# Performance work log

Hardware: AMD Instinct MI355X
Metric: run time of the kernel (lower is better)

Reference implementation:

```python
import jax, jax.numpy as jnp
import numpy as np

UNITS = 65
BATCH = 50
SEQ = 8192


def setup_inputs() -> dict:
    key = jax.random.key(0)
    ks = jax.random.split(key, 6)
    x = jax.random.normal(ks[0], (BATCH, SEQ, UNITS), dtype=jnp.float32)
    # Single shared LSTM cell (same cell object reused for all 3 stacked layers)
    W = jax.random.normal(ks[1], (UNITS, 4 * UNITS), dtype=jnp.float32) * 0.1
    U = jax.random.normal(ks[2], (UNITS, 4 * UNITS), dtype=jnp.float32) * 0.1
    b = jax.random.normal(ks[3], (4 * UNITS,), dtype=jnp.float32) * 0.1
    # Dense output projection 65 -> 65
    Wd = jax.random.normal(ks[4], (UNITS, UNITS), dtype=jnp.float32) * 0.1
    bd = jax.random.normal(ks[5], (UNITS,), dtype=jnp.float32) * 0.1
    return {"x": x, "W": W, "U": U, "b": b, "Wd": Wd, "bd": bd}


def _lstm_cell(x_t, h, c, W, U, b):
    # Keras LSTMCell: gates in order i, f, g(candidate), o
    z = x_t @ W + h @ U + b                      # [B, 4*units]
    i, f, g, o = jnp.split(z, 4, axis=-1)
    i = jax.nn.sigmoid(i)
    f = jax.nn.sigmoid(f)
    g = jnp.tanh(g)
    o = jax.nn.sigmoid(o)
    c_new = f * c + i * g
    h_new = o * jnp.tanh(c_new)
    return h_new, c_new


def reference(x, W, U, b, Wd, bd):
    B = x.shape[0]
    zeros = jnp.zeros((B, UNITS), dtype=x.dtype)
    init = (zeros, zeros, zeros, zeros, zeros, zeros)  # (h1,c1,h2,c2,h3,c3)

    def step(carry, x_t):
        h1, c1, h2, c2, h3, c3 = carry
        h1, c1 = _lstm_cell(x_t, h1, c1, W, U, b)  # layer 1 (shared weights)
        h2, c2 = _lstm_cell(h1, h2, c2, W, U, b)   # layer 2 (shared weights)
        h3, c3 = _lstm_cell(h2, h3, c3, W, U, b)   # layer 3 (shared weights)
        return (h1, c1, h2, c2, h3, c3), h3

    xs = jnp.swapaxes(x, 0, 1)                   # [T, B, 65]
    _, ys = jax.lax.scan(step, init, xs)         # ys: [T, B, 65]
    ys = jnp.swapaxes(ys, 0, 1)                  # [B, T, 65]
    out = ys @ Wd + bd                           # dense projection to vocab 65
    return out
```

## Files before the change

### kernel.cpp

```cpp
#include <hip/hip_runtime.h>

#define UNITS 65
#define SEQ   8192
#define BATCH 50

__device__ __forceinline__ float frcp(float x){ return __builtin_amdgcn_rcpf(x); }
__device__ __forceinline__ float fsigmoid(float x){ return frcp(1.0f + __expf(-x)); }
__device__ __forceinline__ float ftanh(float x){
    float e2 = __expf(2.0f * x);
    return 1.0f - 2.0f * frcp(e2 + 1.0f);
}

template<int CTRL>
__device__ __forceinline__ float dppadd(float x){
    int t = __builtin_amdgcn_update_dpp(0, __float_as_int(x), CTRL, 0xF, 0xF, true);
    return x + __int_as_float(t);
}
template<int CTRL>
__device__ __forceinline__ float dppmov(float x){
    int t = __builtin_amdgcn_update_dpp(0, __float_as_int(x), CTRL, 0xF, 0xF, true);
    return __int_as_float(t);
}
__device__ __forceinline__ float red4_all(float x){
    x = dppadd<0xB1>(x);
    x = dppadd<0x4E>(x);
    return x;
}
__device__ __forceinline__ float red16_lane15(float x){
    x = dppadd<0x111>(x);
    x = dppadd<0x112>(x);
    x = dppadd<0x114>(x);
    x = dppadd<0x118>(x);
    return x;
}
__device__ __forceinline__ void bar_lds(){
    asm volatile("s_waitcnt lgkmcnt(0)\n\ts_barrier" ::: "memory");
}
__device__ __forceinline__ float rdlane(float v, int l){
    return __int_as_float(__builtin_amdgcn_readlane(__float_as_int(v), l));
}

__device__ __forceinline__ int inpos(int k){
    int q = k >> 5; if (q > 3) q = 3;
    return q * 36 + (k - (q << 5));
}
__device__ __forceinline__ float wrow(const float* W, const float* U, int k, int c){
    return (k < 65) ? W[k * 260 + c] : U[(k - 65) * 260 + c];
}


#define LOADVV(vv, base) do {                                                  \
    const float* vp_ = (base) + kq * 36;                                       \
    _Pragma("unroll")                                                          \
    for (int q8_ = 0; q8_ < 8; ++q8_) {                                        \
        float4 f_ = *(const float4*)(vp_ + 4 * q8_);                           \
        vv[4*q8_+0] = f_.x; vv[4*q8_+1] = f_.y;                                \
        vv[4*q8_+2] = f_.z; vv[4*q8_+3] = f_.w;                                \
    }                                                                          \
    { float2 f2_ = *(const float2*)(vp_ + 32); vv[32] = f2_.x; vv[33] = f2_.y; } \
} while (0)

#define LAYERB(aI, aF, aG, aO, CST, ...) do {                                  \
    float rI_ = red4_all(aI), rF_ = red4_all(aF);                              \
    float rG_ = red4_all(aG), rO_ = red4_all(aO);                              \
    float z_ = ((kq == 0) ? rI_ : (kq == 1) ? rF_ : (kq == 2) ? rG_ : rO_) + breg; \
    float sg_ = frcp(1.0f + __expf(-sk * z_));                                 \
    float g_  = fmaf(sk, sg_, dk);                                             \
    float gi_ = dppmov<0x00>(g_);                                              \
    float gf_ = dppmov<0x55>(g_);                                              \
    float gg_ = dppmov<0xAA>(g_);                                              \
    float cn_ = fmaf(gf_, CST, gi_ * gg_);                                     \
    float hn_ = g_ * ftanh(cn_);                                               \
    if (wr) { CST = cn_; __VA_ARGS__; }                                        \
} while (0)

#define STEP(L0, L1, L2) do {                                                  \
    const float* __restrict__ vbase = &vbuf[cur][0][0];                        \
    float*       __restrict__ nbase = &vbuf[cur ^ 1][0][0];                    \
         \
    float xq1 = 0.0f, ex1 = 0.0f;                                              \
    if (L0) {                                                                  \
        const int tl_ = (s + 2 < SEQ) ? (s + 2) : (SEQ - 1);                   \
        if (wr) xq1 = xrow[(size_t)tl_ * UNITS + j];                           \
        if (wave == 1 && lane == 0) ex1 = xrow[(size_t)tl_ * UNITS + 64];      \
    }                                                                          \
            \
    float vv0[34], vv1[34], vv2[34];                                           \
    if (L0) LOADVV(vv0, vbase);                                                \
    if (L1) LOADVV(vv1, vbase + 144);                                          \
    if (L2) LOADVV(vv2, vbase + 288);                                          \
        \
    const float* vm_ = vbase + ml * 144;                                       \
    float4 uA_ = *(const float4*)(vm_ + p64);                                  \
    float4 uB_ = *(const float4*)(vm_ + p64 + 4);                              \
    float  uex_ = (i64 < 2) ? vm_[140 + i64] : 0.0f;                           \
                   \
    float aI0=0,aF0=0,aG0=0,aO0=0, aI1=0,aF1=0,aG1=0,aO1=0,                    \
          aI2=0,aF2=0,aG2=0,aO2=0;                                             \
    _Pragma("unroll")                                                          \
    for (int kk = 0; kk < 34; ++kk) {                                          \
        if (L0) { float s0_ = vv0[kk];                                         \
            aI0=fmaf(s0_,wI[kk],aI0); aF0=fmaf(s0_,wF[kk],aF0);                \
            aG0=fmaf(s0_,wG[kk],aG0); aO0=fmaf(s0_,wO[kk],aO0); }              \
        if (L1) { float s1_ = vv1[kk];                                         \
            aI1=fmaf(s1_,wI[kk],aI1); aF1=fmaf(s1_,wF[kk],aF1);                \
            aG1=fmaf(s1_,wG[kk],aG1); aO1=fmaf(s1_,wO[kk],aO1); }              \
        if (L2) { float s2_ = vv2[kk];                                         \
            aI2=fmaf(s2_,wI[kk],aI2); aF2=fmaf(s2_,wF[kk],aF2);                \
            aG2=fmaf(s2_,wG[kk],aG2); aO2=fmaf(s2_,wO[kk],aO2); }              \
    }                                                                          \
                           \
    float a64_ = uA_.x * w64[0];                                               \
    a64_ = fmaf(uA_.y, w64[1], a64_); a64_ = fmaf(uA_.z, w64[2], a64_);        \
    a64_ = fmaf(uA_.w, w64[3], a64_); a64_ = fmaf(uB_.x, w64[4], a64_);        \
    a64_ = fmaf(uB_.y, w64[5], a64_); a64_ = fmaf(uB_.z, w64[6], a64_);        \
    a64_ = fmaf(uB_.w, w64[7], a64_); a64_ = fmaf(uex_, w64x, a64_);           \
    a64_ = red16_lane15(a64_);                                                 \
                                            \
    if (L0) LAYERB(aI0, aF0, aG0, aO0, c1,                                     \
                   nbase[ipH] = hn_; nbase[144 + ipI] = hn_);                  \
    if (L1) LAYERB(aI1, aF1, aG1, aO1, c2,                                     \
                   nbase[144 + ipH] = hn_; nbase[288 + ipI] = hn_);            \
    if (L2) LAYERB(aI2, aF2, aG2, aO2, c3,                                     \
                   nbase[288 + ipH] = hn_;                                     \
                   orow[(size_t)(s - 2) * UNITS + j] = hn_);                   \
    if (L0) { if (wr) { nbase[ipI] = xq0; xq0 = xq1; } }                       \
                               \
    {                                                                          \
        const bool act64_ = (wave == 1) ? (bool)(L0)                           \
                          : (wave == 2) ? (bool)(L1)                           \
                          : (wave == 3) ? (bool)(L2) : false;                  \
        float zi_ = rdlane(a64_, 15) + b64i;                                   \
        float zf_ = rdlane(a64_, 31) + b64f;                                   \
        float zg_ = rdlane(a64_, 47) + b64g;                                   \
        float zo_ = rdlane(a64_, 63) + b64o;                                   \
        float gi4_ = fsigmoid(zi_), gf4_ = fsigmoid(zf_);                      \
        float gg4_ = ftanh(zg_),    go4_ = fsigmoid(zo_);                      \
        float cn64_ = fmaf(gf4_, c64, gi4_ * gg4_);                            \
        float hn64_ = go4_ * ftanh(cn64_);                                     \
        if (act64_) {                                                          \
            c64 = cn64_;                                                       \
            if (lane == 0) {                                                   \
                nbase[ml * 144 + 141] = hn64_;                                 \
                if (wave <= 2) nbase[wave * 144 + 72] = hn64_;                 \
                else orow[(size_t)(s - 2) * UNITS + 64] = hn64_;               \
            }                                                                  \
            if (wave == 1) { if (lane == 0) nbase[72] = ex0; ex0 = ex1; }      \
        }                                                                      \
    }                                                                          \
    cur ^= 1;                                                                  \
    bar_lds();                                                                 \
} while (0)

__global__ __launch_bounds__(256, 1)
void lstm3_kernel(const float* __restrict__ x, const float* __restrict__ W,
                  const float* __restrict__ U, const float* __restrict__ b,
                  float* __restrict__ out)
{
    const int e    = blockIdx.x;
    const int tid  = threadIdx.x;
    const int wave = tid >> 6, lane = tid & 63;
    const int kq   = lane & 3, jl = lane >> 2;
    const int j    = wave * 16 + jl;
    const bool wr  = (kq == 3);

    __shared__ __attribute__((aligned(16))) float vbuf[2][3][144];

    float wI[34], wF[34], wG[34], wO[34];
    #pragma unroll
    for (int kk = 0; kk < 34; ++kk) {
        int k = kq * 32 + kk;
        wI[kk] = wrow(W, U, k, j);
        wF[kk] = wrow(W, U, k, 65  + j);
        wG[kk] = wrow(W, U, k, 130 + j);
        wO[kk] = wrow(W, U, k, 195 + j);
    }
    const float breg = b[kq * 65 + j];
    const float sk   = (kq == 2) ? 2.0f : 1.0f;
    const float dk   = 1.0f - sk;

    const int i64 = lane & 15, g64 = lane >> 4;
    const int p64 = (i64 >> 2) * 36 + 8 * (i64 & 3);
    float w64[8], w64x;
    {
        const int c64 = g64 * 65 + 64;
        #pragma unroll
        for (int r = 0; r < 8; ++r) w64[r] = wrow(W, U, 8 * i64 + r, c64);
        w64x = (i64 < 2) ? wrow(W, U, 128 + i64, c64) : 0.0f;
    }
    const float b64i = b[64], b64f = b[129], b64g = b[194], b64o = b[259];
    const int ml = (wave == 0) ? 0 : wave - 1;

    float c1 = 0, c2 = 0, c3 = 0, c64 = 0;

    const float* xrow = x   + (size_t)e * SEQ * UNITS;
    float*       orow = out + (size_t)e * SEQ * UNITS;
    const int ipI = inpos(j), ipH = inpos(65 + j);

    for (int i = tid; i < 2 * 3 * 144; i += 256) ((float*)vbuf)[i] = 0.0f;
    __syncthreads();
    if (wr)  vbuf[0][0][ipI] = xrow[j];
    if (wave == 1 && lane == 0) vbuf[0][0][72] = xrow[64];
    __syncthreads();

    float xq0 = 0, ex0 = 0;
    if (wr) xq0 = xrow[UNITS + j];
    if (wave == 1 && lane == 0) ex0 = xrow[UNITS + 64];

    int cur = 0;
    int s = 0;
    STEP(1, 0, 0); ++s;
    STEP(1, 1, 0); ++s;
    for (; s < SEQ; ++s) { STEP(1, 1, 1); }
    STEP(0, 1, 1); ++s;
    STEP(0, 0, 1);
}

__global__ __launch_bounds__(256)
void dense_kernel(float* __restrict__ io,
                  const float* __restrict__ Wd,
                  const float* __restrict__ bd)
{
    __shared__ __attribute__((aligned(16))) float wS[65 * 68];
    __shared__ float bS[65];
    for (int i = threadIdx.x; i < 65 * 65; i += 256) {
        int r = i / 65, c = i - r * 65;
        wS[r * 68 + c] = Wd[i];
    }
    if (threadIdx.x < 65) bS[threadIdx.x] = bd[threadIdx.x];
    __syncthreads();

    const size_t row  = (size_t)blockIdx.x * 256 + threadIdx.x;
    const size_t base = row * 65;

    float r[65];
    #pragma unroll
    for (int k = 0; k < 65; ++k) r[k] = io[base + k];

    for (int ct = 0; ct < 16; ++ct) {
        const int c = ct * 4;
        float a0 = bS[c], a1 = bS[c + 1], a2 = bS[c + 2], a3 = bS[c + 3];
        #pragma unroll
        for (int k = 0; k < 65; ++k) {
            const float4 wv = *reinterpret_cast<const float4*>(&wS[k * 68 + c]);
            a0 += r[k] * wv.x;
            a1 += r[k] * wv.y;
            a2 += r[k] * wv.z;
            a3 += r[k] * wv.w;
        }
        io[base + c]     = a0;
        io[base + c + 1] = a1;
        io[base + c + 2] = a2;
        io[base + c + 3] = a3;
    }
    float a = bS[64];
    #pragma unroll
    for (int k = 0; k < 65; ++k) a += r[k] * wS[k * 68 + 64];
    io[base + 64] = a;
}

extern "C" void kernel_launch(void* const* d_in, const int* in_sizes, int n_in,
                              void* d_out, int out_size, void* d_ws, size_t ws_size,
                              hipStream_t stream)
{
    const float* x  = (const float*)d_in[0];
    const float* W  = (const float*)d_in[1];
    const float* U  = (const float*)d_in[2];
    const float* b  = (const float*)d_in[3];
    const float* Wd = (const float*)d_in[4];
    const float* bd = (const float*)d_in[5];
    float* out = (float*)d_out;

    hipLaunchKernelGGL(lstm3_kernel, dim3(BATCH), dim3(256), 0, stream, x, W, U, b, out);
    hipLaunchKernelGGL(dense_kernel, dim3(1600), dim3(256), 0, stream, out, Wd, bd);
}
```

Before: 15.23 ms.

## Pack two batch sequences per 512-thread block and stream LDS loads into FMA loop

Each block now runs two independent batch elements, eight waves sharing one barrier, with separate LDS double buffers per element. The grid is halved to 25 blocks. The per-step vector loads are moved inside the FMA loop as float4 chunks instead of being staged into 34-element register arrays, which cuts register pressure so two waves fit per SIMD. The cost is that each barrier now waits on both sequences, and launch_bounds(512,2) may force register spills given the ~136 weight registers per thread.

```diff
diff --git a/kernel.cpp b/kernel.cpp
--- a/kernel.cpp
+++ b/kernel.cpp
@@ -48,17 +48,6 @@
     return (k < 65) ? W[k * 260 + c] : U[(k - 65) * 260 + c];
 }
 
-
-#define LOADVV(vv, base) do {                                                  \
-    const float* vp_ = (base) + kq * 36;                                       \
-    _Pragma("unroll")                                                          \
-    for (int q8_ = 0; q8_ < 8; ++q8_) {                                        \
-        float4 f_ = *(const float4*)(vp_ + 4 * q8_);                           \
-        vv[4*q8_+0] = f_.x; vv[4*q8_+1] = f_.y;                                \
-        vv[4*q8_+2] = f_.z; vv[4*q8_+3] = f_.w;                                \
-    }                                                                          \
-    { float2 f2_ = *(const float2*)(vp_ + 32); vv[32] = f2_.x; vv[33] = f2_.y; } \
-} while (0)
 
 #define LAYERB(aI, aF, aG, aO, CST, ...) do {                                  \
     float rI_ = red4_all(aI), rF_ = red4_all(aF);                              \
@@ -75,39 +64,64 @@
 } while (0)
 
 #define STEP(L0, L1, L2) do {                                                  \
-    const float* __restrict__ vbase = &vbuf[cur][0][0];                        \
-    float*       __restrict__ nbase = &vbuf[cur ^ 1][0][0];                    \
-         \
+    const float* __restrict__ vbase = &vbuf[eh][cur][0][0];                    \
+    float*       __restrict__ nbase = &vbuf[eh][cur ^ 1][0][0];                \
+           \
     float xq1 = 0.0f, ex1 = 0.0f;                                              \
     if (L0) {                                                                  \
         const int tl_ = (s + 2 < SEQ) ? (s + 2) : (SEQ - 1);                   \
         if (wr) xq1 = xrow[(size_t)tl_ * UNITS + j];                           \
-        if (wave == 1 && lane == 0) ex1 = xrow[(size_t)tl_ * UNITS + 64];      \
-    }                                                                          \
-            \
-    float vv0[34], vv1[34], vv2[34];                                           \
-    if (L0) LOADVV(vv0, vbase);                                                \
-    if (L1) LOADVV(vv1, vbase + 144);                                          \
-    if (L2) LOADVV(vv2, vbase + 288);                                          \
-        \
+        if (wave4 == 1 && lane == 0) ex1 = xrow[(size_t)tl_ * UNITS + 64];     \
+    }                                                                          \
+     \
     const float* vm_ = vbase + ml * 144;                                       \
     float4 uA_ = *(const float4*)(vm_ + p64);                                  \
     float4 uB_ = *(const float4*)(vm_ + p64 + 4);                              \
     float  uex_ = (i64 < 2) ? vm_[140 + i64] : 0.0f;                           \
-                   \
+     \
+    const float* vp0_ = vbase + kq * 36;                                       \
+    const float* vp1_ = vbase + 144 + kq * 36;                                 \
+    const float* vp2_ = vbase + 288 + kq * 36;                                 \
     float aI0=0,aF0=0,aG0=0,aO0=0, aI1=0,aF1=0,aG1=0,aO1=0,                    \
           aI2=0,aF2=0,aG2=0,aO2=0;                                             \
     _Pragma("unroll")                                                          \
-    for (int kk = 0; kk < 34; ++kk) {                                          \
-        if (L0) { float s0_ = vv0[kk];                                         \
-            aI0=fmaf(s0_,wI[kk],aI0); aF0=fmaf(s0_,wF[kk],aF0);                \
-            aG0=fmaf(s0_,wG[kk],aG0); aO0=fmaf(s0_,wO[kk],aO0); }              \
-        if (L1) { float s1_ = vv1[kk];                                         \
-            aI1=fmaf(s1_,wI[kk],aI1); aF1=fmaf(s1_,wF[kk],aF1);                \
-            aG1=fmaf(s1_,wG[kk],aG1); aO1=fmaf(s1_,wO[kk],aO1); }              \
-        if (L2) { float s2_ = vv2[kk];                                         \
-            aI2=fmaf(s2_,wI[kk],aI2); aF2=fmaf(s2_,wF[kk],aF2);                \
-            aG2=fmaf(s2_,wG[kk],aG2); aO2=fmaf(s2_,wO[kk],aO2); }              \
+    for (int q8_ = 0; q8_ < 8; ++q8_) {                                        \
+        float4 f0_, f1_, f2_;                                                  \
+        if (L0) f0_ = *(const float4*)(vp0_ + 4 * q8_);                        \
+        if (L1) f1_ = *(const float4*)(vp1_ + 4 * q8_);                        \
+        if (L2) f2_ = *(const float4*)(vp2_ + 4 * q8_);                        \
+        _Pragma("unroll")                                                      \
+        for (int r_ = 0; r_ < 4; ++r_) {                                       \
+            const int kk = 4 * q8_ + r_;                                       \
+            if (L0) { float s0_ = (&f0_.x)[r_];                                \
+                aI0=fmaf(s0_,wI[kk],aI0); aF0=fmaf(s0_,wF[kk],aF0);            \
+                aG0=fmaf(s0_,wG[kk],aG0); aO0=fmaf(s0_,wO[kk],aO0); }          \
+            if (L1) { float s1_ = (&f1_.x)[r_];                                \
+                aI1=fmaf(s1_,wI[kk],aI1); aF1=fmaf(s1_,wF[kk],aF1);            \
+                aG1=fmaf(s1_,wG[kk],aG1); aO1=fmaf(s1_,wO[kk],aO1); }          \
+            if (L2) { float s2_ = (&f2_.x)[r_];                                \
+                aI2=fmaf(s2_,wI[kk],aI2); aF2=fmaf(s2_,wF[kk],aF2);            \
+                aG2=fmaf(s2_,wG[kk],aG2); aO2=fmaf(s2_,wO[kk],aO2); }          \
+        }                                                                      \
+    }                                                                          \
+    {                                                     \
+        float2 t0_, t1_, t2_;                                                  \
+        if (L0) t0_ = *(const float2*)(vp0_ + 32);                             \
+        if (L1) t1_ = *(const float2*)(vp1_ + 32);                             \
+        if (L2) t2_ = *(const float2*)(vp2_ + 32);                             \
+        _Pragma("unroll")                                                      \
+        for (int r_ = 0; r_ < 2; ++r_) {                                       \
+            const int kk = 32 + r_;                                            \
+            if (L0) { float s0_ = (&t0_.x)[r_];                                \
+                aI0=fmaf(s0_,wI[kk],aI0); aF0=fmaf(s0_,wF[kk],aF0);            \
+                aG0=fmaf(s0_,wG[kk],aG0); aO0=fmaf(s0_,wO[kk],aO0); }          \
+            if (L1) { float s1_ = (&t1_.x)[r_];                                \
+                aI1=fmaf(s1_,wI[kk],aI1); aF1=fmaf(s1_,wF[kk],aF1);            \
+                aG1=fmaf(s1_,wG[kk],aG1); aO1=fmaf(s1_,wO[kk],aO1); }          \
+            if (L2) { float s2_ = (&t2_.x)[r_];                                \
+                aI2=fmaf(s2_,wI[kk],aI2); aF2=fmaf(s2_,wF[kk],aF2);            \
+                aG2=fmaf(s2_,wG[kk],aG2); aO2=fmaf(s2_,wO[kk],aO2); }          \
+        }                                                                      \
     }                                                                          \
                            \
     float a64_ = uA_.x * w64[0];                                               \
@@ -127,9 +141,9 @@
     if (L0) { if (wr) { nbase[ipI] = xq0; xq0 = xq1; } }                       \
                                \
     {                                                                          \
-        const bool act64_ = (wave == 1) ? (bool)(L0)                           \
-                          : (wave == 2) ? (bool)(L1)                           \
-                          : (wave == 3) ? (bool)(L2) : false;                  \
+        const bool act64_ = (wave4 == 1) ? (bool)(L0)                          \
+                          : (wave4 == 2) ? (bool)(L1)                          \
+                          : (wave4 == 3) ? (bool)(L2) : false;                 \
         float zi_ = rdlane(a64_, 15) + b64i;                                   \
         float zf_ = rdlane(a64_, 31) + b64f;                                   \
         float zg_ = rdlane(a64_, 47) + b64g;                                   \
@@ -142,29 +156,30 @@
             c64 = cn64_;                                                       \
             if (lane == 0) {                                                   \
                 nbase[ml * 144 + 141] = hn64_;                                 \
-                if (wave <= 2) nbase[wave * 144 + 72] = hn64_;                 \
+                if (wave4 <= 2) nbase[wave4 * 144 + 72] = hn64_;               \
                 else orow[(size_t)(s - 2) * UNITS + 64] = hn64_;               \
             }                                                                  \
-            if (wave == 1) { if (lane == 0) nbase[72] = ex0; ex0 = ex1; }      \
+            if (wave4 == 1) { if (lane == 0) nbase[72] = ex0; ex0 = ex1; }     \
         }                                                                      \
     }                                                                          \
     cur ^= 1;                                                                  \
     bar_lds();                                                                 \
 } while (0)
 
-__global__ __launch_bounds__(256, 1)
+__global__ __launch_bounds__(512, 2)
 void lstm3_kernel(const float* __restrict__ x, const float* __restrict__ W,
                   const float* __restrict__ U, const float* __restrict__ b,
                   float* __restrict__ out)
 {
-    const int e    = blockIdx.x;
-    const int tid  = threadIdx.x;
-    const int wave = tid >> 6, lane = tid & 63;
-    const int kq   = lane & 3, jl = lane >> 2;
-    const int j    = wave * 16 + jl;
-    const bool wr  = (kq == 3);
-
-    __shared__ __attribute__((aligned(16))) float vbuf[2][3][144];
+    const int tid   = threadIdx.x;
+    const int wave  = tid >> 6, lane = tid & 63;
+    const int eh    = wave >> 2, wave4 = wave & 3;
+    const int e     = blockIdx.x * 2 + eh;
+    const int kq    = lane & 3, jl = lane >> 2;
+    const int j     = wave4 * 16 + jl;
+    const bool wr   = (kq == 3);
+
+    __shared__ __attribute__((aligned(16))) float vbuf[2][2][3][144];
 
     float wI[34], wF[34], wG[34], wO[34];
     #pragma unroll
@@ -189,7 +204,7 @@
         w64x = (i64 < 2) ? wrow(W, U, 128 + i64, c64) : 0.0f;
     }
     const float b64i = b[64], b64f = b[129], b64g = b[194], b64o = b[259];
-    const int ml = (wave == 0) ? 0 : wave - 1;
+    const int ml = (wave4 == 0) ? 0 : wave4 - 1;
 
     float c1 = 0, c2 = 0, c3 = 0, c64 = 0;
 
@@ -197,15 +212,15 @@
     float*       orow = out + (size_t)e * SEQ * UNITS;
     const int ipI = inpos(j), ipH = inpos(65 + j);
 
-    for (int i = tid; i < 2 * 3 * 144; i += 256) ((float*)vbuf)[i] = 0.0f;
+    for (int i = tid; i < 2 * 2 * 3 * 144; i += 512) ((float*)&vbuf[0][0][0][0])[i] = 0.0f;
     __syncthreads();
-    if (wr)  vbuf[0][0][ipI] = xrow[j];
-    if (wave == 1 && lane == 0) vbuf[0][0][72] = xrow[64];
+    if (wr)  vbuf[eh][0][0][ipI] = xrow[j];
+    if (wave4 == 1 && lane == 0) vbuf[eh][0][0][72] = xrow[64];
     __syncthreads();
 
     float xq0 = 0, ex0 = 0;
     if (wr) xq0 = xrow[UNITS + j];
-    if (wave == 1 && lane == 0) ex0 = xrow[UNITS + 64];
+    if (wave4 == 1 && lane == 0) ex0 = xrow[UNITS + 64];
 
     int cur = 0;
     int s = 0;
@@ -271,6 +286,6 @@
     const float* bd = (const float*)d_in[5];
     float* out = (float*)d_out;
 
-    hipLaunchKernelGGL(lstm3_kernel, dim3(BATCH), dim3(256), 0, stream, x, W, U, b, out);
+    hipLaunchKernelGGL(lstm3_kernel, dim3(BATCH / 2), dim3(512), 0, stream, x, W, U, b, out);
     hipLaunchKernelGGL(dense_kernel, dim3(1600), dim3(256), 0, stream, out, Wd, bd);
 }
```

Result: slower. 23.89 ms (+56.8%).

## Give each lane a full gate column and broadcast inputs via readlane

Applied to the files above, without the earlier changes.

The gate matmul is reorganised so each lane owns one gate column and keeps all 130 weights in registers. The state vector is read from LDS as one float4 per lane and broadcast with v_readlane, instead of each lane loading 34 values and reducing four partial sums with DPP. The x prefetch and the 65th unit's computation are restructured to match the new LDS layout. This removes the per-lane LDS vector loads and the cross-lane reductions. In exchange it adds about one readlane per FMA, lengthens the dependent FMA chains and raises register pressure.

```diff
diff --git a/kernel.cpp b/kernel.cpp
--- a/kernel.cpp
+++ b/kernel.cpp
@@ -3,6 +3,8 @@
 #define UNITS 65
 #define SEQ   8192
 #define BATCH 50
+#define LW    136
+#define PW    (3 * LW)
 
 __device__ __forceinline__ float frcp(float x){ return __builtin_amdgcn_rcpf(x); }
 __device__ __forceinline__ float fsigmoid(float x){ return frcp(1.0f + __expf(-x)); }
@@ -21,131 +23,115 @@
     int t = __builtin_amdgcn_update_dpp(0, __float_as_int(x), CTRL, 0xF, 0xF, true);
     return __int_as_float(t);
 }
-__device__ __forceinline__ float red4_all(float x){
-    x = dppadd<0xB1>(x);
-    x = dppadd<0x4E>(x);
-    return x;
-}
-__device__ __forceinline__ float red16_lane15(float x){
+__device__ __forceinline__ float red64_63(float x){
     x = dppadd<0x111>(x);
     x = dppadd<0x112>(x);
     x = dppadd<0x114>(x);
     x = dppadd<0x118>(x);
+    x = dppadd<0x142>(x);
+    x = dppadd<0x143>(x);
     return x;
 }
 __device__ __forceinline__ void bar_lds(){
     asm volatile("s_waitcnt lgkmcnt(0)\n\ts_barrier" ::: "memory");
 }
-__device__ __forceinline__ float rdlane(float v, int l){
-    return __int_as_float(__builtin_amdgcn_readlane(__float_as_int(v), l));
-}
-
-__device__ __forceinline__ int inpos(int k){
-    int q = k >> 5; if (q > 3) q = 3;
-    return q * 36 + (k - (q << 5));
-}
+
 __device__ __forceinline__ float wrow(const float* W, const float* U, int k, int c){
     return (k < 65) ? W[k * 260 + c] : U[(k - 65) * 260 + c];
 }
 
-
-#define LOADVV(vv, base) do {                                                  \
-    const float* vp_ = (base) + kq * 36;                                       \
-    _Pragma("unroll")                                                          \
-    for (int q8_ = 0; q8_ < 8; ++q8_) {                                        \
-        float4 f_ = *(const float4*)(vp_ + 4 * q8_);                           \
-        vv[4*q8_+0] = f_.x; vv[4*q8_+1] = f_.y;                                \
-        vv[4*q8_+2] = f_.z; vv[4*q8_+3] = f_.w;                                \
-    }                                                                          \
-    { float2 f2_ = *(const float2*)(vp_ + 32); vv[32] = f2_.x; vv[33] = f2_.y; } \
-} while (0)
-
-#define LAYERB(aI, aF, aG, aO, CST, ...) do {                                  \
-    float rI_ = red4_all(aI), rF_ = red4_all(aF);                              \
-    float rG_ = red4_all(aG), rO_ = red4_all(aO);                              \
-    float z_ = ((kq == 0) ? rI_ : (kq == 1) ? rF_ : (kq == 2) ? rG_ : rO_) + breg; \
+#define VW(K) ((K) < 65 ? (K) : (K) + 3)
+#define RLF(fv, W_) __int_as_float(__builtin_amdgcn_readlane(                   \
+        __float_as_int((&(fv).x)[(W_) & 3]), (W_) >> 2))
+
+
+#define ACT(ZS, CST, ...) do {                                                 \
+    float z_  = (ZS) + breg;                                                   \
     float sg_ = frcp(1.0f + __expf(-sk * z_));                                 \
-    float g_  = fmaf(sk, sg_, dk);                                             \
+    float g_  = fmaf(sk, sg_, dk);            \
     float gi_ = dppmov<0x00>(g_);                                              \
     float gf_ = dppmov<0x55>(g_);                                              \
     float gg_ = dppmov<0xAA>(g_);                                              \
     float cn_ = fmaf(gf_, CST, gi_ * gg_);                                     \
     float hn_ = g_ * ftanh(cn_);                                               \
-    if (wr) { CST = cn_; __VA_ARGS__; }                                        \
+    if (og) { CST = cn_; __VA_ARGS__; }                                        \
 } while (0)
 
 #define STEP(L0, L1, L2) do {                                                  \
-    const float* __restrict__ vbase = &vbuf[cur][0][0];                        \
-    float*       __restrict__ nbase = &vbuf[cur ^ 1][0][0];                    \
-         \
-    float xq1 = 0.0f, ex1 = 0.0f;                                              \
-    if (L0) {                                                                  \
+    float* vb = lds + cur * PW;                                                \
+    float* vn = lds + (cur ^ 1) * PW;                                          \
+              \
+    float4 nx4 = {0,0,0,0}; float nxs = 0.0f;                                  \
+    if (L0) { if (wave == 0) {                                                 \
         const int tl_ = (s + 2 < SEQ) ? (s + 2) : (SEQ - 1);                   \
-        if (wr) xq1 = xrow[(size_t)tl_ * UNITS + j];                           \
-        if (wave == 1 && lane == 0) ex1 = xrow[(size_t)tl_ * UNITS + 64];      \
+        if (lane < 16) nx4 = *(const float4*)(xrow + (size_t)tl_ * UNITS + 4 * lane); \
+        if (lane == 16) nxs = xrow[(size_t)tl_ * UNITS + 64];                  \
+    } }                                                                        \
+                           \
+    float4 fv0 = {0,0,0,0}, fv1 = {0,0,0,0}, fv2 = {0,0,0,0};                  \
+    if (L0) fv0 = *(const float4*)(vb + rdoff);                                \
+    if (L1) fv1 = *(const float4*)(vb + LW + rdoff);                           \
+    if (L2) fv2 = *(const float4*)(vb + 2 * LW + rdoff);                       \
+     \
+    float a0 = 0, a0b = 0, a1 = 0, a1b = 0, a2 = 0, a2b = 0;                   \
+    _Pragma("unroll")                                                          \
+    for (int k = 0; k < 130; ++k) {                                            \
+        if (L0) { float sv_ = RLF(fv0, VW(k));                                 \
+            if (k < 65) a0  = fmaf(sv_, wcol[k], a0);                          \
+            else        a0b = fmaf(sv_, wcol[k], a0b); }                       \
+        if (L1) { float sv_ = RLF(fv1, VW(k));                                 \
+            if (k < 65) a1  = fmaf(sv_, wcol[k], a1);                          \
+            else        a1b = fmaf(sv_, wcol[k], a1b); }                       \
+        if (L2) { float sv_ = RLF(fv2, VW(k));                                 \
+            if (k < 65) a2  = fmaf(sv_, wcol[k], a2);                          \
+            else        a2b = fmaf(sv_, wcol[k], a2b); }                       \
     }                                                                          \
-            \
-    float vv0[34], vv1[34], vv2[34];                                           \
-    if (L0) LOADVV(vv0, vbase);                                                \
-    if (L1) LOADVV(vv1, vbase + 144);                                          \
-    if (L2) LOADVV(vv2, vbase + 288);                                          \
-        \
-    const float* vm_ = vbase + ml * 144;                                       \
-    float4 uA_ = *(const float4*)(vm_ + p64);                                  \
-    float4 uB_ = *(const float4*)(vm_ + p64 + 4);                              \
-    float  uex_ = (i64 < 2) ? vm_[140 + i64] : 0.0f;                           \
-                   \
-    float aI0=0,aF0=0,aG0=0,aO0=0, aI1=0,aF1=0,aG1=0,aO1=0,                    \
-          aI2=0,aF2=0,aG2=0,aO2=0;                                             \
-    _Pragma("unroll")                                                          \
-    for (int kk = 0; kk < 34; ++kk) {                                          \
-        if (L0) { float s0_ = vv0[kk];                                         \
-            aI0=fmaf(s0_,wI[kk],aI0); aF0=fmaf(s0_,wF[kk],aF0);                \
-            aG0=fmaf(s0_,wG[kk],aG0); aO0=fmaf(s0_,wO[kk],aO0); }              \
-        if (L1) { float s1_ = vv1[kk];                                         \
-            aI1=fmaf(s1_,wI[kk],aI1); aF1=fmaf(s1_,wF[kk],aF1);                \
-            aG1=fmaf(s1_,wG[kk],aG1); aO1=fmaf(s1_,wO[kk],aO1); }              \
-        if (L2) { float s2_ = vv2[kk];                                         \
-            aI2=fmaf(s2_,wI[kk],aI2); aF2=fmaf(s2_,wF[kk],aF2);                \
-            aG2=fmaf(s2_,wG[kk],aG2); aO2=fmaf(s2_,wO[kk],aO2); }              \
-    }                                                                          \
-                           \
-    float a64_ = uA_.x * w64[0];                                               \
-    a64_ = fmaf(uA_.y, w64[1], a64_); a64_ = fmaf(uA_.z, w64[2], a64_);        \
-    a64_ = fmaf(uA_.w, w64[3], a64_); a64_ = fmaf(uB_.x, w64[4], a64_);        \
-    a64_ = fmaf(uB_.y, w64[5], a64_); a64_ = fmaf(uB_.z, w64[6], a64_);        \
-    a64_ = fmaf(uB_.w, w64[7], a64_); a64_ = fmaf(uex_, w64x, a64_);           \
-    a64_ = red16_lane15(a64_);                                                 \
-                                            \
-    if (L0) LAYERB(aI0, aF0, aG0, aO0, c1,                                     \
-                   nbase[ipH] = hn_; nbase[144 + ipI] = hn_);                  \
-    if (L1) LAYERB(aI1, aF1, aG1, aO1, c2,                                     \
-                   nbase[144 + ipH] = hn_; nbase[288 + ipI] = hn_);            \
-    if (L2) LAYERB(aI2, aF2, aG2, aO2, c3,                                     \
-                   nbase[288 + ipH] = hn_;                                     \
-                   orow[(size_t)(s - 2) * UNITS + j] = hn_);                   \
-    if (L0) { if (wr) { nbase[ipI] = xq0; xq0 = xq1; } }                       \
-                               \
+           \
+    if (L0) { if (wave == 0) {                                                 \
+        if (lane < 16) *(float4*)(vn + 4 * lane) = xq4;                        \
+        if (lane == 16) vn[64] = xqs;                                          \
+        xq4 = nx4; xqs = nxs;                                                  \
+    } }                                                                        \
+                                                   \
+    if (L0) ACT(a0 + a0b, c_0,                                                 \
+                vn[68 + j] = hn_;                         \
+                vn[LW + j] = hn_);                        \
+    if (L1) ACT(a1 + a1b, c_1,                                                 \
+                vn[LW + 68 + j] = hn_;                                         \
+                vn[2 * LW + j] = hn_);                                         \
+    if (L2) ACT(a2 + a2b, c_2,                                                 \
+                vn[2 * LW + 68 + j] = hn_;                                     \
+                orow[(size_t)(s - 2) * UNITS + j] = hn_);                      \
+                          \
     {                                                                          \
-        const bool act64_ = (wave == 1) ? (bool)(L0)                           \
-                          : (wave == 2) ? (bool)(L1)                           \
-                          : (wave == 3) ? (bool)(L2) : false;                  \
-        float zi_ = rdlane(a64_, 15) + b64i;                                   \
-        float zf_ = rdlane(a64_, 31) + b64f;                                   \
-        float zg_ = rdlane(a64_, 47) + b64g;                                   \
-        float zo_ = rdlane(a64_, 63) + b64o;                                   \
-        float gi4_ = fsigmoid(zi_), gf4_ = fsigmoid(zf_);                      \
-        float gg4_ = ftanh(zg_),    go4_ = fsigmoid(zo_);                      \
-        float cn64_ = fmaf(gf4_, c64, gi4_ * gg4_);                            \
-        float hn64_ = go4_ * ftanh(cn64_);                                     \
-        if (act64_) {                                                          \
-            c64 = cn64_;                                                       \
-            if (lane == 0) {                                                   \
-                nbase[ml * 144 + 141] = hn64_;                                 \
-                if (wave <= 2) nbase[wave * 144 + 72] = hn64_;                 \
+        const bool a64_ = (wave == 1) ? (bool)(L0)                             \
+                        : (wave == 2) ? (bool)(L1)                             \
+                        : (wave == 3) ? (bool)(L2) : false;                    \
+        if (a64_) {                                                            \
+            float4 fvm = (m64 == 0) ? fv0 : (m64 == 1) ? fv1 : fv2;            \
+            float p0 = 0, p1 = 0, p2 = 0, p3 = 0;                              \
+            _Pragma("unroll")                                                  \
+            for (int i = 0; i < 4; ++i) {                                      \
+                float sv_ = (&fvm.x)[i];                                       \
+                p0 = fmaf(sv_, w64w[i][0], p0);                                \
+                p1 = fmaf(sv_, w64w[i][1], p1);                                \
+                p2 = fmaf(sv_, w64w[i][2], p2);                                \
+                p3 = fmaf(sv_, w64w[i][3], p3);                                \
+            }                                                                  \
+            p0 = red64_63(p0); p1 = red64_63(p1);                              \
+            p2 = red64_63(p2); p3 = red64_63(p3);                              \
+            float gi4_ = fsigmoid(p0 + b64i);                                  \
+            float gf4_ = fsigmoid(p1 + b64f);                                  \
+            float gg4_ = ftanh  (p2 + b64g);                                   \
+            float go4_ = fsigmoid(p3 + b64o);                                  \
+            float cn64_ = fmaf(gf4_, c64, gi4_ * gg4_);                        \
+            float hn64_ = go4_ * ftanh(cn64_);                                 \
+            if (lane == 63) {                                                  \
+                c64 = cn64_;                                                   \
+                vn[m64 * LW + 132] = hn64_;                   \
+                if (wave <= 2) vn[(m64 + 1) * LW + 64] = hn64_;                \
                 else orow[(size_t)(s - 2) * UNITS + 64] = hn64_;               \
             }                                                                  \
-            if (wave == 1) { if (lane == 0) nbase[72] = ex0; ex0 = ex1; }      \
         }                                                                      \
     }                                                                          \
     cur ^= 1;                                                                  \
@@ -160,52 +146,56 @@
     const int e    = blockIdx.x;
     const int tid  = threadIdx.x;
     const int wave = tid >> 6, lane = tid & 63;
-    const int kq   = lane & 3, jl = lane >> 2;
-    const int j    = wave * 16 + jl;
-    const bool wr  = (kq == 3);
-
-    __shared__ __attribute__((aligned(16))) float vbuf[2][3][144];
-
-    float wI[34], wF[34], wG[34], wO[34];
-    #pragma unroll
-    for (int kk = 0; kk < 34; ++kk) {
-        int k = kq * 32 + kk;
-        wI[kk] = wrow(W, U, k, j);
-        wF[kk] = wrow(W, U, k, 65  + j);
-        wG[kk] = wrow(W, U, k, 130 + j);
-        wO[kk] = wrow(W, U, k, 195 + j);
-    }
-    const float breg = b[kq * 65 + j];
-    const float sk   = (kq == 2) ? 2.0f : 1.0f;
+    const int u    = lane >> 2;
+    const int gate = lane & 3;
+    const int j    = wave * 16 + u;
+    const bool og  = (gate == 3);
+
+    __shared__ __attribute__((aligned(16))) float lds[2 * PW];
+
+    float wcol[130];
+    #pragma unroll
+    for (int k = 0; k < 130; ++k) wcol[k] = wrow(W, U, k, gate * 65 + j);
+    #pragma unroll
+    for (int k = 0; k < 130; ++k) { asm volatile("" : "+v"(wcol[k])); }
+
+    const float breg = b[gate * 65 + j];
+    const float sk   = (gate == 2) ? 2.0f : 1.0f;
     const float dk   = 1.0f - sk;
 
-    const int i64 = lane & 15, g64 = lane >> 4;
-    const int p64 = (i64 >> 2) * 36 + 8 * (i64 & 3);
-    float w64[8], w64x;
-    {
-        const int c64 = g64 * 65 + 64;
+    const int rdoff = (lane < 34) ? 4 * lane : 132;
+
+    const int m64 = (wave >= 1) ? (wave - 1) : 0;
+    float w64w[4][4];
+    #pragma unroll
+    for (int i = 0; i < 4; ++i) {
+        const int  wd  = rdoff + i;
+        const bool val = (wave >= 1) && (lane < 34) &&
+                         !(wd >= 65 && wd < 68) && (wd < 133);
+        const int  k   = (wd < 65) ? wd : wd - 3;
         #pragma unroll
-        for (int r = 0; r < 8; ++r) w64[r] = wrow(W, U, 8 * i64 + r, c64);
-        w64x = (i64 < 2) ? wrow(W, U, 128 + i64, c64) : 0.0f;
+        for (int g = 0; g < 4; ++g)
+            w64w[i][g] = val ? wrow(W, U, k, g * 65 + 64) : 0.0f;
     }
     const float b64i = b[64], b64f = b[129], b64g = b[194], b64o = b[259];
-    const int ml = (wave == 0) ? 0 : wave - 1;
-
-    float c1 = 0, c2 = 0, c3 = 0, c64 = 0;
+
+    float c_0 = 0, c_1 = 0, c_2 = 0, c64 = 0;
 
     const float* xrow = x   + (size_t)e * SEQ * UNITS;
     float*       orow = out + (size_t)e * SEQ * UNITS;
-    const int ipI = inpos(j), ipH = inpos(65 + j);
-
-    for (int i = tid; i < 2 * 3 * 144; i += 256) ((float*)vbuf)[i] = 0.0f;
+
+    for (int i = tid; i < 2 * PW; i += 256) lds[i] = 0.0f;
     __syncthreads();
-    if (wr)  vbuf[0][0][ipI] = xrow[j];
-    if (wave == 1 && lane == 0) vbuf[0][0][72] = xrow[64];
+    if (wave == 0) {
+        if (lane < 16) *(float4*)(lds + 4 * lane) = *(const float4*)(xrow + 4 * lane);
+        if (lane == 16) lds[64] = xrow[64];
+    }
     __syncthreads();
-
-    float xq0 = 0, ex0 = 0;
-    if (wr) xq0 = xrow[UNITS + j];
-    if (wave == 1 && lane == 0) ex0 = xrow[UNITS + 64];
+    float4 xq4 = {0,0,0,0}; float xqs = 0.0f;
+    if (wave == 0) {
+        if (lane < 16) xq4 = *(const float4*)(xrow + UNITS + 4 * lane);
+        if (lane == 16) xqs = xrow[UNITS + 64];
+    }
 
     int cur = 0;
     int s = 0;
```

Result: slower. 41.05 ms (+169.5%).
